# Performance work log

Measured on AMD Instinct MI355X. Metric: run time of the kernel, lower is better.

Reference implementation:

```python
import jax, jax.numpy as jnp
import numpy as np

B, T = 32, 1024
IN0 = 512   # 2 * hidden_dim
H = 256     # input_dim // 2


def _lstm_layer(x, Wih, Whh, bih, bhh):
    """Single unidirectional LSTM layer, PyTorch gate order (i, f, g, o).
    x: [B, T, D] -> returns h sequence [B, T, H]."""
    # Precompute the input projection for all timesteps in one big GEMM.
    xg = jnp.einsum('btd,gd->btg', x, Wih) + bih + bhh  # [B, T, 4H]
    xg = jnp.swapaxes(xg, 0, 1)                          # [T, B, 4H]

    h0 = jnp.zeros((x.shape[0], H), x.dtype)
    c0 = jnp.zeros((x.shape[0], H), x.dtype)

    def step(carry, xg_t):
        h, c = carry
        gates = xg_t + h @ Whh.T            # [B, 4H]
        i, f, g, o = jnp.split(gates, 4, axis=-1)
        i = jax.nn.sigmoid(i)
        f = jax.nn.sigmoid(f)
        g = jnp.tanh(g)
        o = jax.nn.sigmoid(o)
        c = f * c + i * g
        h = o * jnp.tanh(c)
        return (h, c), h

    (_, _), hs = jax.lax.scan(step, (h0, c0), xg)  # hs: [T, B, H]
    return jnp.swapaxes(hs, 0, 1)                  # [B, T, H]


def setup_inputs() -> dict:
    key = jax.random.key(0)
    ks = jax.random.split(key, 9)
    s = 1.0 / np.sqrt(H)  # torch LSTM init scale
    u = lambda k, shp: jax.random.uniform(k, shp, jnp.float32, -s, s)
    return {
        'encoder_outputs': jax.random.normal(ks[0], (B, T, IN0), jnp.float32),
        'Wih0': u(ks[1], (4 * H, IN0)),
        'Whh0': u(ks[2], (4 * H, H)),
        'bih0': u(ks[3], (4 * H,)),
        'bhh0': u(ks[4], (4 * H,)),
        'Wih1': u(ks[5], (4 * H, H)),
        'Whh1': u(ks[6], (4 * H, H)),
        'bih1': u(ks[7], (4 * H,)),
        'bhh1': u(ks[8], (4 * H,)),
    }


def reference(encoder_outputs, Wih0, Whh0, bih0, bhh0, Wih1, Whh1, bih1, bhh1):
    h1 = _lstm_layer(encoder_outputs, Wih0, Whh0, bih0, bhh0)
    # dropout=0.0 between layers (eval-mode math)
    h2 = _lstm_layer(h1, Wih1, Whh1, bih1, bhh1)
    return h2  # [B, T, H] reconstruction
```

## Files before the change

### kernel.cpp

```cpp
#include <hip/hip_runtime.h>

#define BATCH 32
#define TFULL 1024
#define HDIM  256
#define G4    1024
#define TC    128
#define NWG   512

__global__ __launch_bounds__(512) void gemm_xg(
    const float* __restrict__ X, const float* __restrict__ W,
    const float* __restrict__ bia, const float* __restrict__ bib,
    float* __restrict__ xg, int K, int trows, int t0)
{
  __shared__ float Xs[16][128];
  __shared__ float Ws[16][128];
  const int tid = threadIdx.x;
  const int m0 = blockIdx.x * 128;
  const int n0 = blockIdx.y * 128;
  const int tx = tid & 15;
  const int ty = tid >> 4;

  float acc[4][8];
#pragma unroll
  for (int i = 0; i < 4; ++i)
#pragma unroll
    for (int j = 0; j < 8; ++j) acc[i][j] = 0.f;

  const int r  = tid >> 2;
  const int kq = tid & 3;
  const int m  = m0 + r;
  const int bX = m & 31;
  const int tl = m >> 5;
  const float* xrow = X + (bX * trows + t0 + tl) * K;
  const float* wrow = W + (n0 + r) * K;

  for (int kt = 0; kt < K; kt += 16) {
    float4 xv = *(const float4*)&xrow[kt + kq * 4];
    float4 wv = *(const float4*)&wrow[kt + kq * 4];
    Xs[kq * 4 + 0][r] = xv.x; Xs[kq * 4 + 1][r] = xv.y;
    Xs[kq * 4 + 2][r] = xv.z; Xs[kq * 4 + 3][r] = xv.w;
    Ws[kq * 4 + 0][r] = wv.x; Ws[kq * 4 + 1][r] = wv.y;
    Ws[kq * 4 + 2][r] = wv.z; Ws[kq * 4 + 3][r] = wv.w;
    __syncthreads();
#pragma unroll
    for (int k = 0; k < 16; ++k) {
      float4 xa = *(const float4*)&Xs[k][ty * 4];
      float4 wa = *(const float4*)&Ws[k][tx * 8];
      float4 wb = *(const float4*)&Ws[k][tx * 8 + 4];
      float xr[4] = {xa.x, xa.y, xa.z, xa.w};
      float wr[8] = {wa.x, wa.y, wa.z, wa.w, wb.x, wb.y, wb.z, wb.w};
#pragma unroll
      for (int i = 0; i < 4; ++i)
#pragma unroll
        for (int j = 0; j < 8; ++j)
          acc[i][j] = fmaf(xr[i], wr[j], acc[i][j]);
    }
    __syncthreads();
  }

  float bb[8];
#pragma unroll
  for (int j = 0; j < 8; ++j) {
    int n = n0 + tx * 8 + j;
    bb[j] = bia[n] + bib[n];
  }
#pragma unroll
  for (int i = 0; i < 4; ++i) {
    int mm = m0 + ty * 4 + i;
    int b = mm & 31, t = mm >> 5;
    float* dst = &xg[(size_t)(t * BATCH + b) * G4 + n0 + tx * 8];
    float4 v0 = make_float4(acc[i][0] + bb[0], acc[i][1] + bb[1],
                            acc[i][2] + bb[2], acc[i][3] + bb[3]);
    float4 v1 = make_float4(acc[i][4] + bb[4], acc[i][5] + bb[5],
                            acc[i][6] + bb[6], acc[i][7] + bb[7]);
    *(float4*)dst = v0;
    *(float4*)(dst + 4) = v1;
  }
}

#define PIN_LOAD16(W, PTR)                                             \
  asm volatile(                                                        \
      "global_load_dwordx4 %0,  %16, off\n\t"                          \
      "global_load_dwordx4 %1,  %16, off offset:16\n\t"                \
      "global_load_dwordx4 %2,  %16, off offset:32\n\t"                \
      "global_load_dwordx4 %3,  %16, off offset:48\n\t"                \
      "global_load_dwordx4 %4,  %16, off offset:64\n\t"                \
      "global_load_dwordx4 %5,  %16, off offset:80\n\t"                \
      "global_load_dwordx4 %6,  %16, off offset:96\n\t"                \
      "global_load_dwordx4 %7,  %16, off offset:112\n\t"               \
      "global_load_dwordx4 %8,  %16, off offset:128\n\t"               \
      "global_load_dwordx4 %9,  %16, off offset:144\n\t"               \
      "global_load_dwordx4 %10, %16, off offset:160\n\t"               \
      "global_load_dwordx4 %11, %16, off offset:176\n\t"               \
      "global_load_dwordx4 %12, %16, off offset:192\n\t"               \
      "global_load_dwordx4 %13, %16, off offset:208\n\t"               \
      "global_load_dwordx4 %14, %16, off offset:224\n\t"               \
      "global_load_dwordx4 %15, %16, off offset:240\n\t"               \
      "s_waitcnt vmcnt(0)"                                             \
      : "=&v"(W[0]), "=&v"(W[1]), "=&v"(W[2]), "=&v"(W[3]),            \
        "=&v"(W[4]), "=&v"(W[5]), "=&v"(W[6]), "=&v"(W[7]),            \
        "=&v"(W[8]), "=&v"(W[9]), "=&v"(W[10]), "=&v"(W[11]),          \
        "=&v"(W[12]), "=&v"(W[13]), "=&v"(W[14]), "=&v"(W[15])         \
      : "v"(PTR) : "memory")

#define DOT64(A0, A1, A2, A3, WREG, HP)                                \
  _Pragma("unroll")                                                    \
  for (int q = 0; q < 16; q += 4) {                                    \
    float4 h0 = (HP)[q+0], h1q = (HP)[q+1];                            \
    float4 h2 = (HP)[q+2], h3q = (HP)[q+3];                            \
    A0 = fmaf(WREG[q+0].x, h0.x, A0);  A0 = fmaf(WREG[q+0].y, h0.y, A0);  \
    A0 = fmaf(WREG[q+0].z, h0.z, A0);  A0 = fmaf(WREG[q+0].w, h0.w, A0);  \
    A1 = fmaf(WREG[q+1].x, h1q.x, A1); A1 = fmaf(WREG[q+1].y, h1q.y, A1); \
    A1 = fmaf(WREG[q+1].z, h1q.z, A1); A1 = fmaf(WREG[q+1].w, h1q.w, A1); \
    A2 = fmaf(WREG[q+2].x, h2.x, A2);  A2 = fmaf(WREG[q+2].y, h2.y, A2);  \
    A2 = fmaf(WREG[q+2].z, h2.z, A2);  A2 = fmaf(WREG[q+2].w, h2.w, A2);  \
    A3 = fmaf(WREG[q+3].x, h3q.x, A3); A3 = fmaf(WREG[q+3].y, h3q.y, A3); \
    A3 = fmaf(WREG[q+3].z, h3q.z, A3); A3 = fmaf(WREG[q+3].w, h3q.w, A3); \
  }

#define POLL_MB(G, OUT_A, OUT_B, SPTR)                                 \
  {                                                                    \
    for (;;) {                                                         \
      asm volatile(                                                    \
          "global_load_dwordx4 %0, %2, off sc0 sc1\n\t"                \
          "global_load_dwordx4 %1, %3, off sc0 sc1\n\t"                \
          "s_waitcnt vmcnt(0)"                                         \
          : "=&v"(OUT_A), "=&v"(OUT_B)                                 \
          : "v"(SPTR), "v"((SPTR) + 1) : "memory");                    \
      bool ok = (__float_as_uint(OUT_A.y) == (G)) &&                   \
                (__float_as_uint(OUT_A.w) == (G)) &&                   \
                (__float_as_uint(OUT_B.y) == (G)) &&                   \
                (__float_as_uint(OUT_B.w) == (G));                     \
      if (__all(ok)) break;                                            \
    }                                                                  \
  }

__global__ __launch_bounds__(256, 2) void lstm_scan2(
    const float* __restrict__ xg0,
    const float* __restrict__ Whh0,
    const float* __restrict__ Wih1,
    const float* __restrict__ Whh1,
    const float* __restrict__ bih1, const float* __restrict__ bhh1,
    float* __restrict__ out,
    float* __restrict__ mbA,
    float* __restrict__ mbB,
    float* __restrict__ cbA,
    float* __restrict__ cbB,
    int T0, int niter, int nL0)
{
  const int w    = blockIdx.x;
  const int tid  = threadIdx.x;
  const int s    = w & 31;
  const int r    = w >> 5;
  const int gt   = tid >> 6;
  const int lane = tid & 63;
  const int jl   = lane & 15;
  const int kq   = lane >> 4;
  const int n    = gt * 256 + r * 16 + jl;

  __shared__ float hA[HDIM];
  __shared__ float hB[HDIM];
  __shared__ float part0[64];
  __shared__ float part1[64];

  float4 w0[16], w1[16], wi[16];
  {
    const float4* p0 = (const float4*)(Whh0 + (size_t)n * HDIM + kq * 64);
    const float4* p1 = (const float4*)(Whh1 + (size_t)n * HDIM + kq * 64);
    const float4* pi = (const float4*)(Wih1 + (size_t)n * HDIM + kq * 64);
    PIN_LOAD16(w0, p0);
    PIN_LOAD16(w1, p1);
    PIN_LOAD16(wi, pi);
  }
  const float b1 = bih1[n] + bhh1[n];

  float cA_reg = 0.f, cB_reg = 0.f;
  if (tid < 16)                cA_reg = cbA[s * HDIM + r * 16 + tid];
  if (tid >= 64 && tid < 80)   cB_reg = cbB[s * HDIM + r * 16 + (tid - 64)];

  float* mA = mbA + (size_t)s * 8 * 512;
  float* mB = mbB + (size_t)s * 8 * 512;

  for (int i = 0; i < niter; ++i) {
    const int t = T0 + i;
    const bool doL0 = (i < nL0);
    const bool doL1 = (t > 0);
    const unsigned gA = (unsigned)t;
    const unsigned gB = (unsigned)(t - 1);

    float xv = 0.f;
    if (doL0) xv = xg0[((size_t)(i * BATCH + s) << 10) + n];

    if (tid < 64) {
      const float4* sp = (const float4*)(mA + (size_t)(gA & 7) * 512) + tid * 2;
      float4 A, Bq;
      POLL_MB(gA, A, Bq, sp);
      *(float4*)&hA[tid * 4] = make_float4(A.x, A.z, Bq.x, Bq.z);
    } else if (tid < 128 && doL1) {
      const int l = tid - 64;
      const float4* sp = (const float4*)(mB + (size_t)(gB & 7) * 512) + l * 2;
      float4 A, Bq;
      POLL_MB(gB, A, Bq, sp);
      *(float4*)&hB[l * 4] = make_float4(A.x, A.z, Bq.x, Bq.z);
    }
    __syncthreads();

    if (doL0) {
      const float4* hp = (const float4*)&hA[kq * 64];
      float a0 = 0.f, a1 = 0.f, a2 = 0.f, a3 = 0.f;
      DOT64(a0, a1, a2, a3, w0, hp);
      float a = (a0 + a1) + (a2 + a3);
      a += __shfl_xor(a, 16);
      a += __shfl_xor(a, 32);
      if (kq == 0) part0[gt * 16 + jl] = a + xv;
    }
    __syncthreads();

    if (doL0 && tid < 16) {
      float gi = part0[tid],      gf = part0[16 + tid];
      float gg = part0[32 + tid], go = part0[48 + tid];
      float ig = 1.f / (1.f + __expf(-gi));
      float fg = 1.f / (1.f + __expf(-gf));
      float gv = tanhf(gg);
      float og = 1.f / (1.f + __expf(-go));
      cA_reg = fg * cA_reg + ig * gv;
      float h = og * tanhf(cA_reg);
      float2 pv; pv.x = h; pv.y = __uint_as_float((unsigned)(t + 1));
      float* pp = mA + (size_t)((t + 1) & 7) * 512 + (r * 16 + tid) * 2;
      asm volatile("global_store_dwordx2 %0, %1, off sc0 sc1"
                   :: "v"(pp), "v"(pv) : "memory");
    }

    if (doL1) {
      const float4* ha = (const float4*)&hA[kq * 64];
      const float4* hb = (const float4*)&hB[kq * 64];
      float a0 = 0.f, a1 = 0.f, a2 = 0.f, a3 = 0.f;
      DOT64(a0, a1, a2, a3, wi, ha);
      DOT64(a0, a1, a2, a3, w1, hb);
      float a = (a0 + a1) + (a2 + a3);
      a += __shfl_xor(a, 16);
      a += __shfl_xor(a, 32);
      if (kq == 0) part1[gt * 16 + jl] = a + b1;
    }
    __syncthreads();

    if (doL1 && tid >= 64 && tid < 80) {
      const int l = tid - 64;
      float gi = part1[l],      gf = part1[16 + l];
      float gg = part1[32 + l], go = part1[48 + l];
      float ig = 1.f / (1.f + __expf(-gi));
      float fg = 1.f / (1.f + __expf(-gf));
      float gv = tanhf(gg);
      float og = 1.f / (1.f + __expf(-go));
      cB_reg = fg * cB_reg + ig * gv;
      float h = og * tanhf(cB_reg);
      float2 pv; pv.x = h; pv.y = __uint_as_float((unsigned)t);
      float* pp = mB + (size_t)(t & 7) * 512 + (r * 16 + l) * 2;
      asm volatile("global_store_dwordx2 %0, %1, off sc0 sc1"
                   :: "v"(pp), "v"(pv) : "memory");
      out[((size_t)s * TFULL + (t - 1)) * HDIM + r * 16 + l] = h;
    }
  }

  if (tid < 16)              cbA[s * HDIM + r * 16 + tid] = cA_reg;
  if (tid >= 64 && tid < 80) cbB[s * HDIM + r * 16 + (tid - 64)] = cB_reg;
}

extern "C" void kernel_launch(void* const* d_in, const int* in_sizes, int n_in,
                              void* d_out, int out_size, void* d_ws, size_t ws_size,
                              hipStream_t stream) {
  (void)in_sizes; (void)n_in; (void)out_size; (void)ws_size;
  const float* enc  = (const float*)d_in[0];
  const float* Wih0 = (const float*)d_in[1];
  const float* Whh0 = (const float*)d_in[2];
  const float* bih0 = (const float*)d_in[3];
  const float* bhh0 = (const float*)d_in[4];
  const float* Wih1 = (const float*)d_in[5];
  const float* Whh1 = (const float*)d_in[6];
  const float* bih1 = (const float*)d_in[7];
  const float* bhh1 = (const float*)d_in[8];
  float* out = (float*)d_out;

  float* ws  = (float*)d_ws;
  float* xg  = ws;
  float* st  = ws + 4194304;
  float* mbA = st;
  float* mbB = st + 131072;
  float* cbA = st + 262144;
  float* cbB = st + 270336;

  hipMemsetAsync(st, 0, (size_t)278528 * 4, stream);

  for (int ch = 0; ch < 8; ++ch) {
    gemm_xg<<<dim3(32, 8), 512, 0, stream>>>(enc, Wih0, bih0, bhh0, xg,
                                             512, TFULL, ch * TC);
    lstm_scan2<<<NWG, 256, 0, stream>>>(xg, Whh0, Wih1, Whh1, bih1, bhh1,
                                        out, mbA, mbB, cbA, cbB,
                                        ch * TC, (ch == 7) ? TC + 1 : TC, TC);
  }
}
```

Baseline: 3.287 ms.

## Split persistent LSTM scan across twice as many workgroups with LDS-resident Wih1

Doubles the number of persistent workgroups so each owns 8 hidden units instead of 16, cutting per-thread K-slice to 32 and register weight footprint; Wih1 weights move to padded LDS while Whh0/Whh1 stay pinned in registers. Layer-1 mailbox reads are issued early as relaxed atomic loads, overlapping with the layer-0 step, with a polling fallback. Activations switch to an exp-based tanh and stores use 64-bit atomic packed value+generation. Risks more cross-workgroup synchronization traffic and requires all 1024 blocks to be co-resident.

Result: slower. 9.067 ms (+175.8%).

```diff
diff --git a/kernel.cpp b/kernel.cpp
--- a/kernel.cpp
+++ b/kernel.cpp
@@ -5,7 +5,7 @@
 #define HDIM  256
 #define G4    1024
 #define TC    128
-#define NWG   512
+#define NWG   1024
 
 __global__ __launch_bounds__(512) void gemm_xg(
     const float* __restrict__ X, const float* __restrict__ W,
@@ -78,64 +78,37 @@
   }
 }
 
-#define PIN_LOAD16(W, PTR)                                             \
+#define PIN_LOAD8(W, PTR)                                              \
   asm volatile(                                                        \
-      "global_load_dwordx4 %0,  %16, off\n\t"                          \
-      "global_load_dwordx4 %1,  %16, off offset:16\n\t"                \
-      "global_load_dwordx4 %2,  %16, off offset:32\n\t"                \
-      "global_load_dwordx4 %3,  %16, off offset:48\n\t"                \
-      "global_load_dwordx4 %4,  %16, off offset:64\n\t"                \
-      "global_load_dwordx4 %5,  %16, off offset:80\n\t"                \
-      "global_load_dwordx4 %6,  %16, off offset:96\n\t"                \
-      "global_load_dwordx4 %7,  %16, off offset:112\n\t"               \
-      "global_load_dwordx4 %8,  %16, off offset:128\n\t"               \
-      "global_load_dwordx4 %9,  %16, off offset:144\n\t"               \
-      "global_load_dwordx4 %10, %16, off offset:160\n\t"               \
-      "global_load_dwordx4 %11, %16, off offset:176\n\t"               \
-      "global_load_dwordx4 %12, %16, off offset:192\n\t"               \
-      "global_load_dwordx4 %13, %16, off offset:208\n\t"               \
-      "global_load_dwordx4 %14, %16, off offset:224\n\t"               \
-      "global_load_dwordx4 %15, %16, off offset:240\n\t"               \
+      "global_load_dwordx4 %0, %8, off\n\t"                            \
+      "global_load_dwordx4 %1, %8, off offset:16\n\t"                  \
+      "global_load_dwordx4 %2, %8, off offset:32\n\t"                  \
+      "global_load_dwordx4 %3, %8, off offset:48\n\t"                  \
+      "global_load_dwordx4 %4, %8, off offset:64\n\t"                  \
+      "global_load_dwordx4 %5, %8, off offset:80\n\t"                  \
+      "global_load_dwordx4 %6, %8, off offset:96\n\t"                  \
+      "global_load_dwordx4 %7, %8, off offset:112\n\t"                 \
       "s_waitcnt vmcnt(0)"                                             \
       : "=&v"(W[0]), "=&v"(W[1]), "=&v"(W[2]), "=&v"(W[3]),            \
-        "=&v"(W[4]), "=&v"(W[5]), "=&v"(W[6]), "=&v"(W[7]),            \
-        "=&v"(W[8]), "=&v"(W[9]), "=&v"(W[10]), "=&v"(W[11]),          \
-        "=&v"(W[12]), "=&v"(W[13]), "=&v"(W[14]), "=&v"(W[15])         \
+        "=&v"(W[4]), "=&v"(W[5]), "=&v"(W[6]), "=&v"(W[7])             \
       : "v"(PTR) : "memory")
 
-#define DOT64(A0, A1, A2, A3, WREG, HP)                                \
+#define DOT8(ACC, W, HP)                                               \
   _Pragma("unroll")                                                    \
-  for (int q = 0; q < 16; q += 4) {                                    \
-    float4 h0 = (HP)[q+0], h1q = (HP)[q+1];                            \
-    float4 h2 = (HP)[q+2], h3q = (HP)[q+3];                            \
-    A0 = fmaf(WREG[q+0].x, h0.x, A0);  A0 = fmaf(WREG[q+0].y, h0.y, A0);  \
-    A0 = fmaf(WREG[q+0].z, h0.z, A0);  A0 = fmaf(WREG[q+0].w, h0.w, A0);  \
-    A1 = fmaf(WREG[q+1].x, h1q.x, A1); A1 = fmaf(WREG[q+1].y, h1q.y, A1); \
-    A1 = fmaf(WREG[q+1].z, h1q.z, A1); A1 = fmaf(WREG[q+1].w, h1q.w, A1); \
-    A2 = fmaf(WREG[q+2].x, h2.x, A2);  A2 = fmaf(WREG[q+2].y, h2.y, A2);  \
-    A2 = fmaf(WREG[q+2].z, h2.z, A2);  A2 = fmaf(WREG[q+2].w, h2.w, A2);  \
-    A3 = fmaf(WREG[q+3].x, h3q.x, A3); A3 = fmaf(WREG[q+3].y, h3q.y, A3); \
-    A3 = fmaf(WREG[q+3].z, h3q.z, A3); A3 = fmaf(WREG[q+3].w, h3q.w, A3); \
-  }
-
-#define POLL_MB(G, OUT_A, OUT_B, SPTR)                                 \
-  {                                                                    \
-    for (;;) {                                                         \
-      asm volatile(                                                    \
-          "global_load_dwordx4 %0, %2, off sc0 sc1\n\t"                \
-          "global_load_dwordx4 %1, %3, off sc0 sc1\n\t"                \
-          "s_waitcnt vmcnt(0)"                                         \
-          : "=&v"(OUT_A), "=&v"(OUT_B)                                 \
-          : "v"(SPTR), "v"((SPTR) + 1) : "memory");                    \
-      bool ok = (__float_as_uint(OUT_A.y) == (G)) &&                   \
-                (__float_as_uint(OUT_A.w) == (G)) &&                   \
-                (__float_as_uint(OUT_B.y) == (G)) &&                   \
-                (__float_as_uint(OUT_B.w) == (G));                     \
-      if (__all(ok)) break;                                            \
-    }                                                                  \
-  }
-
-__global__ __launch_bounds__(256, 2) void lstm_scan2(
+  for (int q = 0; q < 8; ++q) {                                        \
+    float4 _h = (HP)[q];                                               \
+    ACC = fmaf((W)[q].x, _h.x, ACC); ACC = fmaf((W)[q].y, _h.y, ACC);  \
+    ACC = fmaf((W)[q].z, _h.z, ACC); ACC = fmaf((W)[q].w, _h.w, ACC);  \
+  }
+
+__device__ __forceinline__ float sigm_f(float x) {
+  return 1.f / (1.f + __expf(-x));
+}
+__device__ __forceinline__ float tanh_f(float x) {
+  return 1.f - 2.f / (1.f + __expf(2.f * x));
+}
+
+__global__ __launch_bounds__(256, 4) void lstm_scan2(
     const float* __restrict__ xg0,
     const float* __restrict__ Whh0,
     const float* __restrict__ Wih1,
@@ -154,32 +127,39 @@
   const int r    = w >> 5;
   const int gt   = tid >> 6;
   const int lane = tid & 63;
-  const int jl   = lane & 15;
-  const int kq   = lane >> 4;
-  const int n    = gt * 256 + r * 16 + jl;
-
-  __shared__ float hA[HDIM];
-  __shared__ float hB[HDIM];
-  __shared__ float part0[64];
-  __shared__ float part1[64];
-
-  float4 w0[16], w1[16], wi[16];
+  const int jl   = lane & 7;
+  const int kq   = (lane >> 3) & 7;
+  const int n    = gt * 256 + r * 8 + jl;
+
+  __shared__ float wi_lds[256 * 36];
+  __shared__ float hApad[8 * 36];
+  __shared__ float hBpad[8 * 36];
+  __shared__ float part0[32];
+  __shared__ float part1[32];
+
   {
-    const float4* p0 = (const float4*)(Whh0 + (size_t)n * HDIM + kq * 64);
-    const float4* p1 = (const float4*)(Whh1 + (size_t)n * HDIM + kq * 64);
-    const float4* pi = (const float4*)(Wih1 + (size_t)n * HDIM + kq * 64);
-    PIN_LOAD16(w0, p0);
-    PIN_LOAD16(w1, p1);
-    PIN_LOAD16(wi, pi);
-  }
-  const float b1 = bih1[n] + bhh1[n];
-
-  float cA_reg = 0.f, cB_reg = 0.f;
-  if (tid < 16)                cA_reg = cbA[s * HDIM + r * 16 + tid];
-  if (tid >= 64 && tid < 80)   cB_reg = cbB[s * HDIM + r * 16 + (tid - 64)];
+    const float4* src = (const float4*)(Wih1 + (size_t)n * HDIM + kq * 32);
+    float4* dst = (float4*)&wi_lds[tid * 36];
+#pragma unroll
+    for (int q = 0; q < 8; ++q) dst[q] = src[q];
+  }
+
+  float4 w0q[8], w1q[8];
+  {
+    const float4* p0 = (const float4*)(Whh0 + (size_t)n * HDIM + kq * 32);
+    const float4* p1 = (const float4*)(Whh1 + (size_t)n * HDIM + kq * 32);
+    PIN_LOAD8(w0q, p0);
+    PIN_LOAD8(w1q, p1);
+  }
+  const float bs1 = bih1[n] + bhh1[n];
+
+  float cA = 0.f, cB = 0.f;
+  if (tid < 8)               cA = cbA[s * HDIM + r * 8 + tid];
+  if (tid >= 64 && tid < 72) cB = cbB[s * HDIM + r * 8 + (tid - 64)];
 
   float* mA = mbA + (size_t)s * 8 * 512;
   float* mB = mbB + (size_t)s * 8 * 512;
+  __syncthreads();
 
   for (int i = 0; i < niter; ++i) {
     const int t = T0 + i;
@@ -189,81 +169,125 @@
     const unsigned gB = (unsigned)(t - 1);
 
     float xv = 0.f;
-    if (doL0) xv = xg0[((size_t)(i * BATCH + s) << 10) + n];
-
-    if (tid < 64) {
-      const float4* sp = (const float4*)(mA + (size_t)(gA & 7) * 512) + tid * 2;
-      float4 A, Bq;
-      POLL_MB(gA, A, Bq, sp);
-      *(float4*)&hA[tid * 4] = make_float4(A.x, A.z, Bq.x, Bq.z);
-    } else if (tid < 128 && doL1) {
-      const int l = tid - 64;
-      const float4* sp = (const float4*)(mB + (size_t)(gB & 7) * 512) + l * 2;
-      float4 A, Bq;
-      POLL_MB(gB, A, Bq, sp);
-      *(float4*)&hB[l * 4] = make_float4(A.x, A.z, Bq.x, Bq.z);
+    if (doL0 && lane < 8) xv = xg0[((size_t)(i * BATCH + s) << 10) + n];
+
+    unsigned long long bp0 = 0, bp1 = 0;
+    if (tid >= 128 && doL1) {
+      const unsigned long long* bp =
+          (const unsigned long long*)(mB + (size_t)(gB & 7) * 512) +
+          (size_t)(tid - 128) * 2;
+      bp0 = __hip_atomic_load(bp, __ATOMIC_RELAXED, __HIP_MEMORY_SCOPE_AGENT);
+      bp1 = __hip_atomic_load(bp + 1, __ATOMIC_RELAXED,
+                              __HIP_MEMORY_SCOPE_AGENT);
+    }
+
+    if (tid < 128) {
+      const float4* ap = (const float4*)(mA + (size_t)(gA & 7) * 512) + tid;
+      float4 av;
+      for (;;) {
+        asm volatile("global_load_dwordx4 %0, %1, off sc0 sc1\n\t"
+                     "s_waitcnt vmcnt(0)"
+                     : "=&v"(av) : "v"(ap) : "memory");
+        bool ok = (__float_as_uint(av.y) == gA) &&
+                  (__float_as_uint(av.w) == gA);
+        if (__all(ok)) break;
+      }
+      const int c = tid >> 4;
+      const int pos = (2 * tid) & 31;
+      hApad[c * 36 + pos]     = av.x;
+      hApad[c * 36 + pos + 1] = av.z;
     }
     __syncthreads();
 
     if (doL0) {
-      const float4* hp = (const float4*)&hA[kq * 64];
-      float a0 = 0.f, a1 = 0.f, a2 = 0.f, a3 = 0.f;
-      DOT64(a0, a1, a2, a3, w0, hp);
-      float a = (a0 + a1) + (a2 + a3);
+      const float4* hp = (const float4*)&hApad[kq * 36];
+      float a = 0.f;
+      DOT8(a, w0q, hp);
+      a += __shfl_xor(a, 8);
       a += __shfl_xor(a, 16);
       a += __shfl_xor(a, 32);
-      if (kq == 0) part0[gt * 16 + jl] = a + xv;
-    }
-    __syncthreads();
-
-    if (doL0 && tid < 16) {
-      float gi = part0[tid],      gf = part0[16 + tid];
-      float gg = part0[32 + tid], go = part0[48 + tid];
-      float ig = 1.f / (1.f + __expf(-gi));
-      float fg = 1.f / (1.f + __expf(-gf));
-      float gv = tanhf(gg);
-      float og = 1.f / (1.f + __expf(-go));
-      cA_reg = fg * cA_reg + ig * gv;
-      float h = og * tanhf(cA_reg);
-      float2 pv; pv.x = h; pv.y = __uint_as_float((unsigned)(t + 1));
-      float* pp = mA + (size_t)((t + 1) & 7) * 512 + (r * 16 + tid) * 2;
-      asm volatile("global_store_dwordx2 %0, %1, off sc0 sc1"
-                   :: "v"(pp), "v"(pv) : "memory");
-    }
+      if (lane < 8) part0[gt * 8 + jl] = a + xv;
+    }
+    __syncthreads();
+
+    if (doL0 && tid < 8) {
+      float ig = sigm_f(part0[tid]);
+      float fg = sigm_f(part0[8 + tid]);
+      float gv = tanh_f(part0[16 + tid]);
+      float og = sigm_f(part0[24 + tid]);
+      cA = fg * cA + ig * gv;
+      float h = og * tanh_f(cA);
+      unsigned long long pv =
+          ((unsigned long long)(gA + 1u) << 32) |
+          (unsigned long long)__float_as_uint(h);
+      unsigned long long* pp =
+          (unsigned long long*)(mA + (size_t)((gA + 1u) & 7) * 512) +
+          (r * 8 + tid);
+      __hip_atomic_store(pp, pv, __ATOMIC_RELAXED, __HIP_MEMORY_SCOPE_AGENT);
+    }
+
+    if (tid >= 128 && doL1) {
+      const int l2 = tid - 128;
+      float h0, h1;
+      bool ok = ((unsigned)(bp0 >> 32) == gB) && ((unsigned)(bp1 >> 32) == gB);
+      if (__all(ok)) {
+        h0 = __uint_as_float((unsigned)bp0);
+        h1 = __uint_as_float((unsigned)bp1);
+      } else {
+        const float4* bp4 = (const float4*)(mB + (size_t)(gB & 7) * 512) + l2;
+        float4 bv;
+        for (;;) {
+          asm volatile("global_load_dwordx4 %0, %1, off sc0 sc1\n\t"
+                       "s_waitcnt vmcnt(0)"
+                       : "=&v"(bv) : "v"(bp4) : "memory");
+          bool ok2 = (__float_as_uint(bv.y) == gB) &&
+                     (__float_as_uint(bv.w) == gB);
+          if (__all(ok2)) break;
+        }
+        h0 = bv.x; h1 = bv.z;
+      }
+      const int c = l2 >> 4;
+      const int pos = (2 * l2) & 31;
+      hBpad[c * 36 + pos]     = h0;
+      hBpad[c * 36 + pos + 1] = h1;
+    }
+    __syncthreads();
 
     if (doL1) {
-      const float4* ha = (const float4*)&hA[kq * 64];
-      const float4* hb = (const float4*)&hB[kq * 64];
-      float a0 = 0.f, a1 = 0.f, a2 = 0.f, a3 = 0.f;
-      DOT64(a0, a1, a2, a3, wi, ha);
-      DOT64(a0, a1, a2, a3, w1, hb);
-      float a = (a0 + a1) + (a2 + a3);
+      const float4* ha = (const float4*)&hApad[kq * 36];
+      const float4* hb = (const float4*)&hBpad[kq * 36];
+      const float4* wip = (const float4*)&wi_lds[tid * 36];
+      float u = 0.f, v = 0.f;
+      DOT8(u, wip, ha);
+      DOT8(v, w1q, hb);
+      float a = u + v;
+      a += __shfl_xor(a, 8);
       a += __shfl_xor(a, 16);
       a += __shfl_xor(a, 32);
-      if (kq == 0) part1[gt * 16 + jl] = a + b1;
-    }
-    __syncthreads();
-
-    if (doL1 && tid >= 64 && tid < 80) {
+      if (lane < 8) part1[gt * 8 + jl] = a + bs1;
+    }
+    __syncthreads();
+
+    if (doL1 && tid >= 64 && tid < 72) {
       const int l = tid - 64;
-      float gi = part1[l],      gf = part1[16 + l];
-      float gg = part1[32 + l], go = part1[48 + l];
-      float ig = 1.f / (1.f + __expf(-gi));
-      float fg = 1.f / (1.f + __expf(-gf));
-      float gv = tanhf(gg);
-      float og = 1.f / (1.f + __expf(-go));
-      cB_reg = fg * cB_reg + ig * gv;
-      float h = og * tanhf(cB_reg);
-      float2 pv; pv.x = h; pv.y = __uint_as_float((unsigned)t);
-      float* pp = mB + (size_t)(t & 7) * 512 + (r * 16 + l) * 2;
-      asm volatile("global_store_dwordx2 %0, %1, off sc0 sc1"
-                   :: "v"(pp), "v"(pv) : "memory");
-      out[((size_t)s * TFULL + (t - 1)) * HDIM + r * 16 + l] = h;
-    }
-  }
-
-  if (tid < 16)              cbA[s * HDIM + r * 16 + tid] = cA_reg;
-  if (tid >= 64 && tid < 80) cbB[s * HDIM + r * 16 + (tid - 64)] = cB_reg;
+      float ig = sigm_f(part1[l]);
+      float fg = sigm_f(part1[8 + l]);
+      float gv = tanh_f(part1[16 + l]);
+      float og = sigm_f(part1[24 + l]);
+      cB = fg * cB + ig * gv;
+      float h = og * tanh_f(cB);
+      unsigned long long pv =
+          ((unsigned long long)gA << 32) |
+          (unsigned long long)__float_as_uint(h);
+      unsigned long long* pp =
+          (unsigned long long*)(mB + (size_t)(gA & 7) * 512) + (r * 8 + l);
+      __hip_atomic_store(pp, pv, __ATOMIC_RELAXED, __HIP_MEMORY_SCOPE_AGENT);
+      out[((size_t)s * TFULL + (t - 1)) * HDIM + r * 8 + l] = h;
+    }
+  }
+
+  if (tid < 8)               cbA[s * HDIM + r * 8 + tid] = cA;
+  if (tid >= 64 && tid < 72) cbB[s * HDIM + r * 8 + (tid - 64)] = cB;
 }
 
 extern "C" void kernel_launch(void* const* d_in, const int* in_sizes, int n_in,
```
